# Kernel tuning notes

Hardware: AMD Instinct MI355X
Metric: run time of the kernel (lower is better)

Reference implementation:

```python
import jax, jax.numpy as jnp
import numpy as np

# Emulation of MinkowskiEngine sparse conv semantics on a dense grid with an
# occupancy mask: features are zero at unoccupied sites; stride-1 conv outputs
# only at occupied sites (gather-GEMM-scatter over existing coords); stride-2
# maxpool takes max over occupied sites in each 2x2 block and the output site
# is occupied iff any input site was; stride-2 kernel-2 conv-transpose is
# 'generative': each occupied input spawns its full 2x2 output block.
# MinkowskiConvolution has bias=False by default; MinkowskiDropout is identity
# in eval mode (omitted).

_DN = ('NHWC', 'HWIO', 'NHWC')

def mconv(x, m, w):
    # x: [B,H,W,Ci] (zero outside m), m: [B,H,W] bool, w: [kh,kw,Ci,Co]
    y = jax.lax.conv_general_dilated(x, w, (1, 1), 'SAME', dimension_numbers=_DN)
    return jnp.where(m[..., None], y, 0.0)

def mpool(x, m):
    # 2x2 stride-2 max pool over occupied sites only
    B, H, W, C = x.shape
    xn = jnp.where(m[..., None], x, -jnp.inf)
    p = xn.reshape(B, H // 2, 2, W // 2, 2, C).max(axis=(2, 4))
    mo = m.reshape(B, H // 2, 2, W // 2, 2).any(axis=(2, 4))
    return jnp.where(mo[..., None], p, 0.0), mo

def mtconv(x, m, w):
    # kernel-2 stride-2 transpose: out[b,2i+di,2j+dj] = w[di,dj].T @ x[b,i,j]
    B, H, W, Ci = x.shape
    Co = w.shape[-1]
    y = jnp.einsum('bhwc,ijco->bhiwjo', x, w).reshape(B, 2 * H, 2 * W, Co)
    mo = jnp.repeat(jnp.repeat(m, 2, axis=1), 2, axis=2)
    return jnp.where(mo[..., None], y, 0.0), mo


def setup_inputs() -> dict:
    key = jax.random.key(0)
    ks = jax.random.split(key, 20)

    def mkw(k, shape):
        fan_in = int(np.prod(shape[:-1]))
        return (jax.random.normal(k, shape, dtype=jnp.float32) / np.sqrt(fan_in)).astype(jnp.float32)

    B, H, W = 2, 1024, 1024
    x = jax.random.normal(ks[0], (B, H, W, 1), dtype=jnp.float32)
    mask = jax.random.randint(ks[1], (B, H, W), 0, 2, dtype=jnp.int32)
    return {
        'x': x, 'mask': mask,
        'w_ds1': mkw(ks[2], (3, 3, 1, 16)),
        'w_ds2': mkw(ks[3], (3, 3, 16, 32)),
        'w_ds3': mkw(ks[4], (3, 3, 32, 64)),
        'w_ds4': mkw(ks[5], (3, 3, 64, 128)),
        'w_bridge': mkw(ks[6], (3, 3, 128, 256)),
        'wt4': mkw(ks[7], (2, 2, 256, 128)),
        'w_us4': mkw(ks[8], (3, 3, 256, 128)),
        'wt3': mkw(ks[9], (2, 2, 128, 64)),
        'w_us3': mkw(ks[10], (3, 3, 128, 64)),
        'wt2': mkw(ks[11], (2, 2, 64, 32)),
        'w_us2': mkw(ks[12], (3, 3, 64, 32)),
        'wt1': mkw(ks[13], (2, 2, 32, 16)),
        'w_us1': mkw(ks[14], (3, 3, 32, 16)),
        'w_out': mkw(ks[15], (1, 1, 16, 3)),
    }


def reference(x, mask, w_ds1, w_ds2, w_ds3, w_ds4, w_bridge, wt4, w_us4,
              wt3, w_us3, wt2, w_us2, wt1, w_us1, w_out):
    m0 = mask.astype(bool)
    x = jnp.where(m0[..., None], x, 0.0)

    c1 = mconv(x, m0, w_ds1)
    p1, m1 = mpool(c1, m0)
    c2 = mconv(p1, m1, w_ds2)
    p2, m2 = mpool(c2, m1)
    c3 = mconv(p2, m2, w_ds3)
    p3, m3 = mpool(c3, m2)
    c4 = mconv(p3, m3, w_ds4)
    p4, m4 = mpool(c4, m3)

    b = mconv(p4, m4, w_bridge)

    u4, mu4 = mtconv(b, m4, wt4)
    mc4 = mu4 | m3
    r4 = mconv(jnp.concatenate([u4, c4], axis=-1), mc4, w_us4)

    u3, mu3 = mtconv(r4, mc4, wt3)
    mc3 = mu3 | m2
    r3 = mconv(jnp.concatenate([u3, c3], axis=-1), mc3, w_us3)

    u2, mu2 = mtconv(r3, mc3, wt2)
    mc2 = mu2 | m1
    r2 = mconv(jnp.concatenate([u2, c2], axis=-1), mc2, w_us2)

    u1, mu1 = mtconv(r2, mc2, wt1)
    mc1 = mu1 | m0
    r1 = mconv(jnp.concatenate([u1, c1], axis=-1), mc1, w_us1)

    out = mconv(r1, mc1, w_out)
    return (out, c2)
```

## Files before the change

kernel.cpp:

```cpp
#include <hip/hip_runtime.h>
#include <hip/hip_bf16.h>

using bf16 = __hip_bfloat16;
typedef __bf16 bf8 __attribute__((ext_vector_type(8)));
typedef float  f4  __attribute__((ext_vector_type(4)));

__device__ __forceinline__ float b2f(bf16 v){ return __bfloat162float(v); }
__device__ __forceinline__ bf16 f2b(float v){ return __float2bfloat16(v); }

template<typename T> __device__ __forceinline__ float ldv(const void* p, long long i);
template<> __device__ __forceinline__ float ldv<float>(const void* p, long long i){ return ((const float*)p)[i]; }
template<> __device__ __forceinline__ float ldv<bf16 >(const void* p, long long i){ return b2f(((const bf16*)p)[i]); }

__global__ void k_zero_flag(int* f){ *f = 0; }

__global__ void k_detect(const unsigned short* __restrict__ x, long long n, int* __restrict__ flag){
  long long i = blockIdx.x*(long long)blockDim.x + threadIdx.x;
  if (i >= n) return;
  unsigned short u = x[i];
  if ((u & 0x7F80u) == 0x7F80u) atomicOr(flag, 1);
}

__global__ void k_prep(const void* __restrict__ x, const int* __restrict__ m, const int* __restrict__ flag,
                       bf16* __restrict__ xo, unsigned char* __restrict__ mo, long long n){
  long long i = blockIdx.x*(long long)blockDim.x + threadIdx.x;
  if (i >= n) return;
  int f = *flag;
  int mm = (m[i] != 0);
  mo[i] = (unsigned char)mm;
  float v = f ? ldv<float>(x, i) : ldv<bf16>(x, i);
  xo[i] = f2b(mm ? v : 0.f);
}

__global__ void k_mask_comb(const unsigned char* __restrict__ coarse,
                            const unsigned char* __restrict__ fine,
                            unsigned char* __restrict__ mo,
                            int B, int H, int W){
  long long i = blockIdx.x*(long long)blockDim.x + threadIdx.x;
  long long total = (long long)B*H*W;
  if (i >= total) return;
  int x = (int)(i % W);
  long long t = i / W;
  int y = (int)(t % H);
  int b = (int)(t / H);
  unsigned char c = coarse[((long long)b*(H/2) + (y>>1))*(W/2) + (x>>1)];
  mo[i] = (unsigned char)(c | fine[i]);
}

__global__ void k_wt(const int* __restrict__ flag, const void* __restrict__ w, bf16* __restrict__ wt,
                     int taps, int Ci, int Co, int Cip){
  long long i = blockIdx.x*(long long)blockDim.x + threadIdx.x;
  long long total = (long long)taps*Co*Cip;
  if (i >= total) return;
  int ci = (int)(i % Cip);
  long long t2 = i / Cip;
  int co = (int)(t2 % Co);
  int tap = (int)(t2 / Co);
  float v = 0.f;
  if (ci < Ci){
    long long src = ((long long)tap*Ci + ci)*Co + co;
    v = (*flag) ? ldv<float>(w, src) : ldv<bf16>(w, src);
  }
  wt[i] = f2b(v);
}

template<int CI0,int CI1,int CIP,int CO,int COT>
__global__ __launch_bounds__(256)
void k_conv3m(const bf16* __restrict__ in0, const bf16* __restrict__ in1,
              const bf16* __restrict__ wt, const unsigned char* __restrict__ mask,
              void* __restrict__ out, long long out_off, bf16* __restrict__ out2,
              const int* __restrict__ flag, int use_flag,
              int B, int H, int W, int cotiles){
  constexpr int KS = CIP/32;
  int lane = threadIdx.x & 63;
  int wid  = threadIdx.x >> 6;
  int n16  = lane & 15, quad = lane >> 4;
  int x0 = (blockIdx.x*4 + wid)*16;
  int y  = blockIdx.y;
  int b  = blockIdx.z / cotiles;
  int ct = blockIdx.z - b*cotiles;
  int co0 = ct * (16*COT);

  f4 acc[COT];
  #pragma unroll
  for (int j = 0; j < COT; ++j) acc[j] = (f4){0.f,0.f,0.f,0.f};
  bf8 az;
  #pragma unroll
  for (int i = 0; i < 8; ++i) az[i] = (__bf16)0.f;

  bool interior = (x0 > 0) && (x0 + 16 < W);
  int xA = x0 + n16 - 1;

  for (int dy = 0; dy < 3; ++dy){
    int yy = y + dy - 1;
    if ((unsigned)yy >= (unsigned)H) continue;
    const bf16* r0 = in0 + ((long long)b*H + yy)*(long long)W*CI0;
    const bf16* r1 = (CI1 > 0) ? in1 + ((long long)b*H + yy)*(long long)W*CI1 : nullptr;
    const bf16* wrow = wt + ((long long)(dy*3)*CO)*CIP;
    if (interior){
      #pragma unroll
      for (int k0 = 0; k0 < KS; ++k0){
        int c = k0*32 + quad*8;
        bf8 af[3]; bf8 bv[3][COT];
        #pragma unroll
        for (int dx = 0; dx < 3; ++dx){
          long long sx = xA + dx;
          if constexpr (CI1 > 0){
            const bf16* p = (c < CI0) ? r0 + sx*CI0 + c : r1 + sx*CI1 + (c - CI0);
            af[dx] = *(const bf8*)(const void*)p;
          } else if constexpr (CIP > CI0){
            int cc = (c < CI0) ? c : 0;
            bf8 tmp = *(const bf8*)(const void*)(r0 + sx*CI0 + cc);
            af[dx] = (c < CI0) ? tmp : az;
          } else {
            af[dx] = *(const bf8*)(const void*)(r0 + sx*CI0 + c);
          }
          #pragma unroll
          for (int j = 0; j < COT; ++j)
            bv[dx][j] = *(const bf8*)(const void*)(wrow + ((long long)(dx*CO + co0 + j*16 + n16))*CIP + k0*32 + quad*8);
        }
        #pragma unroll
        for (int dx = 0; dx < 3; ++dx)
          #pragma unroll
          for (int j = 0; j < COT; ++j)
            acc[j] = __builtin_amdgcn_mfma_f32_16x16x32_bf16(af[dx], bv[dx][j], acc[j], 0, 0, 0);
      }
    } else {
      #pragma unroll
      for (int k0 = 0; k0 < KS; ++k0){
        int c = k0*32 + quad*8;
        bf8 af[3]; bf8 bv[3][COT];
        #pragma unroll
        for (int dx = 0; dx < 3; ++dx){
          int xx = xA + dx;
          bool ok = (unsigned)xx < (unsigned)W;
          long long sx = ok ? xx : 0;
          bf8 tmp;
          if constexpr (CI1 > 0){
            const bf16* p = (c < CI0) ? r0 + sx*CI0 + c : r1 + sx*CI1 + (c - CI0);
            tmp = *(const bf8*)(const void*)p;
          } else if constexpr (CIP > CI0){
            int cc = (c < CI0) ? c : 0;
            tmp = *(const bf8*)(const void*)(r0 + sx*CI0 + cc);
            if (c >= CI0) ok = false;
          } else {
            tmp = *(const bf8*)(const void*)(r0 + sx*CI0 + c);
          }
          af[dx] = ok ? tmp : az;
          #pragma unroll
          for (int j = 0; j < COT; ++j)
            bv[dx][j] = *(const bf8*)(const void*)(wrow + ((long long)(dx*CO + co0 + j*16 + n16))*CIP + k0*32 + quad*8);
        }
        #pragma unroll
        for (int dx = 0; dx < 3; ++dx)
          #pragma unroll
          for (int j = 0; j < COT; ++j)
            acc[j] = __builtin_amdgcn_mfma_f32_16x16x32_bf16(af[dx], bv[dx][j], acc[j], 0, 0, 0);
      }
    }
  }

  int f = use_flag ? *flag : 0;
  long long srow = ((long long)b*H + y)*(long long)W;
  #pragma unroll
  for (int j = 0; j < COT; ++j){
    #pragma unroll
    for (int r = 0; r < 4; ++r){
      int sx = x0 + quad*4 + r;
      long long s = srow + sx;
      float v = mask[s] ? acc[j][r] : 0.f;
      long long o = s*(long long)CO + co0 + j*16 + n16;
      if (out2) out2[o] = f2b(v);
      if (f) ((float*)out)[out_off + o] = v;
      else   ((bf16*)out)[out_off + o]  = f2b(v);
    }
  }
}

template<int CI,int CO,int COT>
__global__ __launch_bounds__(256)
void k_tconvm(const bf16* __restrict__ in, const bf16* __restrict__ wt,
              bf16* __restrict__ out, int B, int Hi, int Wi, int cotiles){
  constexpr int KS = CI/32;
  int lane = threadIdx.x & 63;
  int wid  = threadIdx.x >> 6;
  int n16  = lane & 15, quad = lane >> 4;
  int ix0 = (blockIdx.x*4 + wid)*16;
  int iy  = blockIdx.y;
  int b   = blockIdx.z / cotiles;
  int ct  = blockIdx.z - b*cotiles;
  int co0 = ct * (16*COT);

  f4 acc[4][COT];
  #pragma unroll
  for (int d = 0; d < 4; ++d)
    #pragma unroll
    for (int j = 0; j < COT; ++j) acc[d][j] = (f4){0.f,0.f,0.f,0.f};

  const bf16* ip = in + (((long long)b*Hi + iy)*(long long)Wi + ix0 + n16)*(long long)CI;
  #pragma unroll
  for (int k0 = 0; k0 < KS; ++k0){
    bf8 a = *(const bf8*)(const void*)(ip + k0*32 + quad*8);
    bf8 bv[4][COT];
    #pragma unroll
    for (int d = 0; d < 4; ++d)
      #pragma unroll
      for (int j = 0; j < COT; ++j)
        bv[d][j] = *(const bf8*)(const void*)(wt + ((long long)(d*CO + co0 + j*16 + n16))*CI + k0*32 + quad*8);
    #pragma unroll
    for (int d = 0; d < 4; ++d)
      #pragma unroll
      for (int j = 0; j < COT; ++j)
        acc[d][j] = __builtin_amdgcn_mfma_f32_16x16x32_bf16(a, bv[d][j], acc[d][j], 0, 0, 0);
  }

  int Ho = Hi*2, Wo = Wi*2;
  #pragma unroll
  for (int d = 0; d < 4; ++d){
    int di = d >> 1, dj = d & 1;
    long long rowo = ((long long)b*Ho + 2*iy + di)*(long long)Wo;
    #pragma unroll
    for (int j = 0; j < COT; ++j){
      #pragma unroll
      for (int r = 0; r < 4; ++r){
        int ix = ix0 + quad*4 + r;
        long long o = (rowo + 2*ix + dj)*(long long)CO + co0 + j*16 + n16;
        out[o] = f2b(acc[d][j][r]);
      }
    }
  }
}

__global__ void k_ds1(const int* __restrict__ flag, const bf16* __restrict__ xm,
                      const void* __restrict__ w, const unsigned char* __restrict__ mask,
                      bf16* __restrict__ out, int B, int H, int W){
  __shared__ float ws[144];
  if (threadIdx.x < 144)
    ws[threadIdx.x] = (*flag) ? ldv<float>(w, threadIdx.x) : ldv<bf16>(w, threadIdx.x);
  __syncthreads();
  long long s = blockIdx.x*(long long)blockDim.x + threadIdx.x;
  long long total = (long long)B*H*W;
  if (s >= total) return;
  int x = (int)(s % W);
  long long t = s / W;
  int y = (int)(t % H);
  int b = (int)(t / H);
  bf8 oz[2];
  #pragma unroll
  for (int h = 0; h < 2; ++h)
    #pragma unroll
    for (int i = 0; i < 8; ++i) oz[h][i] = (__bf16)0.f;
  if (mask[s]){
    float acc[16];
    #pragma unroll
    for (int i = 0; i < 16; ++i) acc[i] = 0.f;
    for (int dy = 0; dy < 3; ++dy){
      int yy = y + dy - 1;
      if ((unsigned)yy >= (unsigned)H) continue;
      long long rowb = ((long long)b*H + yy)*(long long)W;
      for (int dx = 0; dx < 3; ++dx){
        int xx = x + dx - 1;
        if ((unsigned)xx >= (unsigned)W) continue;
        float xv = b2f(xm[rowb + xx]);
        const float* wp = ws + (dy*3 + dx)*16;
        #pragma unroll
        for (int i = 0; i < 16; ++i) acc[i] += xv * wp[i];
      }
    }
    #pragma unroll
    for (int h = 0; h < 2; ++h)
      #pragma unroll
      for (int i = 0; i < 8; ++i) oz[h][i] = (__bf16)acc[h*8+i];
  }
  bf8* op = (bf8*)(void*)(out + s*16);
  op[0] = oz[0]; op[1] = oz[1];
}

__global__ void k_pool8(const bf16* __restrict__ in, const unsigned char* __restrict__ mi,
                        bf16* __restrict__ out, unsigned char* __restrict__ mo,
                        int B, int Ho, int Wo, int C){
  int C8 = C >> 3;
  long long idx = blockIdx.x*(long long)blockDim.x + threadIdx.x;
  long long total = (long long)B*Ho*Wo*C8;
  if (idx >= total) return;
  int c8 = (int)(idx % C8);
  long long s = idx / C8;
  int x = (int)(s % Wo);
  long long t = s / Wo;
  int y = (int)(t % Ho);
  int b = (int)(t / Ho);
  int Hi = Ho*2, Wi = Wo*2;
  float best[8];
  #pragma unroll
  for (int i = 0; i < 8; ++i) best[i] = -3.4e38f;
  bool any = false;
  #pragma unroll
  for (int a = 0; a < 2; ++a){
    #pragma unroll
    for (int d = 0; d < 2; ++d){
      long long site = ((long long)b*Hi + (2*y+a))*(long long)Wi + (2*x+d);
      if (mi[site]){
        any = true;
        bf8 v = *(const bf8*)(const void*)(in + site*(long long)C + c8*8);
        #pragma unroll
        for (int i = 0; i < 8; ++i) best[i] = fmaxf(best[i], (float)v[i]);
      }
    }
  }
  bf8 o;
  #pragma unroll
  for (int i = 0; i < 8; ++i) o[i] = (__bf16)(any ? best[i] : 0.f);
  *(bf8*)(void*)(out + s*(long long)C + c8*8) = o;
  if (c8 == 0) mo[s] = (unsigned char)any;
}

__global__ void k_head(const int* __restrict__ flag, const bf16* __restrict__ in,
                       const void* __restrict__ w, const unsigned char* __restrict__ mask,
                       void* __restrict__ out, int B, int H, int W){
  __shared__ float ws[48];
  if (threadIdx.x < 48)
    ws[threadIdx.x] = (*flag) ? ldv<float>(w, threadIdx.x) : ldv<bf16>(w, threadIdx.x);
  __syncthreads();
  long long s = blockIdx.x*(long long)blockDim.x + threadIdx.x;
  long long total = (long long)B*H*W;
  if (s >= total) return;
  float acc[3] = {0.f, 0.f, 0.f};
  if (mask[s]){
    const bf8* ip = (const bf8*)(const void*)(in + s*16);
    bf8 v0 = ip[0], v1 = ip[1];
    #pragma unroll
    for (int c = 0; c < 8; ++c){
      float a = (float)v0[c], bv = (float)v1[c];
      #pragma unroll
      for (int co = 0; co < 3; ++co){
        acc[co] += a  * ws[c*3 + co];
        acc[co] += bv * ws[(c+8)*3 + co];
      }
    }
  }
  int f = *flag;
  #pragma unroll
  for (int co = 0; co < 3; ++co){
    long long o = s*3 + co;
    if (f) ((float*)out)[o] = acc[co];
    else   ((bf16*)out)[o]  = f2b(acc[co]);
  }
}

static inline dim3 grid1d(long long total, int block){
  return dim3((unsigned)((total + block - 1) / block));
}

extern "C" void kernel_launch(void* const* d_in, const int* in_sizes, int n_in,
                              void* d_out, int out_size, void* d_ws, size_t ws_size,
                              hipStream_t stream) {
  const void* x    = d_in[0];
  const int* mask  = (const int*)d_in[1];
  const void* w_ds1=d_in[2], *w_ds2=d_in[3], *w_ds3=d_in[4], *w_ds4=d_in[5];
  const void* w_bridge=d_in[6];
  const void* wt4=d_in[7], *w_us4=d_in[8], *wt3=d_in[9], *w_us3=d_in[10];
  const void* wt2=d_in[11], *w_us2=d_in[12], *wt1=d_in[13], *w_us1=d_in[14];
  const void* w_out=d_in[15];

  const long long C2_OFF = (long long)2*1024*1024*3;
  const int B = 2;

  int* flag = (int*)d_ws;
  bf16* wsb = (bf16*)((char*)d_ws + 16);
  long long off = 0;
  bf16* xm   = wsb + off; off += (long long)2*1024*1024*1;
  bf16* c1   = wsb + off; off += (long long)2*1024*1024*16;
  bf16* c2b  = wsb + off; off += (long long)2*512*512*32;
  bf16* c3   = wsb + off; off += (long long)2*256*256*64;
  bf16* c4   = wsb + off; off += (long long)2*128*128*128;
  bf16* ping = wsb + off; off += (long long)2*1024*1024*16;
  bf16* pong = wsb + off; off += (long long)2*1024*1024*16;
  bf16* wtds2 = wsb + off; off += (long long)9*32*32;
  bf16* wtds3 = wsb + off; off += (long long)9*64*32;
  bf16* wtds4 = wsb + off; off += (long long)9*128*64;
  bf16* wtbr  = wsb + off; off += (long long)9*256*128;
  bf16* wtus4 = wsb + off; off += (long long)9*128*256;
  bf16* wtus3 = wsb + off; off += (long long)9*64*128;
  bf16* wtus2 = wsb + off; off += (long long)9*32*64;
  bf16* wtus1 = wsb + off; off += (long long)9*16*32;
  bf16* wtt4 = wsb + off; off += (long long)4*128*256;
  bf16* wtt3 = wsb + off; off += (long long)4*64*128;
  bf16* wtt2 = wsb + off; off += (long long)4*32*64;
  bf16* wtt1 = wsb + off; off += (long long)4*16*32;
  unsigned char* mb = (unsigned char*)(wsb + off);
  long long mo = 0;
  unsigned char* m0u = mb + mo; mo += (long long)2*1024*1024;
  unsigned char* m1  = mb + mo; mo += (long long)2*512*512;
  unsigned char* m2  = mb + mo; mo += (long long)2*256*256;
  unsigned char* m3  = mb + mo; mo += (long long)2*128*128;
  unsigned char* m4  = mb + mo; mo += (long long)2*64*64;
  unsigned char* mc4 = mb + mo; mo += (long long)2*128*128;
  unsigned char* mc3 = mb + mo; mo += (long long)2*256*256;
  unsigned char* mc2 = mb + mo; mo += (long long)2*512*512;
  unsigned char* mc1 = mb + mo; mo += (long long)2*1024*1024;

  const int BK = 256;
  long long n;

  k_zero_flag<<<1,1,0,stream>>>(flag);
  n = (long long)B*1024*1024;
  k_detect<<<grid1d(n,BK),BK,0,stream>>>((const unsigned short*)x, n, flag);
  k_prep  <<<grid1d(n,BK),BK,0,stream>>>(x, mask, flag, xm, m0u, n);

  k_wt<<<grid1d((long long)9*32*32 ,BK),BK,0,stream>>>(flag, w_ds2,   wtds2, 9,  16,  32,  32);
  k_wt<<<grid1d((long long)9*64*32 ,BK),BK,0,stream>>>(flag, w_ds3,   wtds3, 9,  32,  64,  32);
  k_wt<<<grid1d((long long)9*128*64,BK),BK,0,stream>>>(flag, w_ds4,   wtds4, 9,  64, 128,  64);
  k_wt<<<grid1d((long long)9*256*128,BK),BK,0,stream>>>(flag, w_bridge,wtbr , 9, 128, 256, 128);
  k_wt<<<grid1d((long long)9*128*256,BK),BK,0,stream>>>(flag, w_us4,  wtus4, 9, 256, 128, 256);
  k_wt<<<grid1d((long long)9*64*128,BK),BK,0,stream>>>(flag, w_us3,   wtus3, 9, 128,  64, 128);
  k_wt<<<grid1d((long long)9*32*64 ,BK),BK,0,stream>>>(flag, w_us2,   wtus2, 9,  64,  32,  64);
  k_wt<<<grid1d((long long)9*16*32 ,BK),BK,0,stream>>>(flag, w_us1,   wtus1, 9,  32,  16,  32);
  k_wt<<<grid1d((long long)4*128*256,BK),BK,0,stream>>>(flag, wt4, wtt4, 4, 256, 128, 256);
  k_wt<<<grid1d((long long)4*64*128 ,BK),BK,0,stream>>>(flag, wt3, wtt3, 4, 128,  64, 128);
  k_wt<<<grid1d((long long)4*32*64  ,BK),BK,0,stream>>>(flag, wt2, wtt2, 4,  64,  32,  64);
  k_wt<<<grid1d((long long)4*16*32  ,BK),BK,0,stream>>>(flag, wt1, wtt1, 4,  32,  16,  32);

  n = (long long)B*1024*1024;
  k_ds1<<<grid1d(n,BK),BK,0,stream>>>(flag, xm, w_ds1, m0u, c1, B,1024,1024);
  n = (long long)B*512*512*2;
  k_pool8<<<grid1d(n,BK),BK,0,stream>>>(c1, m0u, ping, m1, B,512,512,16);

  k_conv3m<16,0,32,32,2><<<dim3(8,512,2),256,0,stream>>>(ping,nullptr, wtds2, m1, d_out, C2_OFF, c2b, flag,1, B,512,512, 1);
  n = (long long)B*256*256*4;
  k_pool8<<<grid1d(n,BK),BK,0,stream>>>(c2b, m1, ping, m2, B,256,256,32);

  k_conv3m<32,0,32,64,2><<<dim3(4,256,4),256,0,stream>>>(ping,nullptr, wtds3, m2, c3, 0, nullptr, flag,0, B,256,256, 2);
  n = (long long)B*128*128*8;
  k_pool8<<<grid1d(n,BK),BK,0,stream>>>(c3, m2, ping, m3, B,128,128,64);

  k_conv3m<64,0,64,128,2><<<dim3(2,128,8),256,0,stream>>>(ping,nullptr, wtds4, m3, c4, 0, nullptr, flag,0, B,128,128, 4);
  n = (long long)B*64*64*16;
  k_pool8<<<grid1d(n,BK),BK,0,stream>>>(c4, m3, ping, m4, B,64,64,128);

  k_conv3m<128,0,128,256,2><<<dim3(1,64,16),256,0,stream>>>(ping,nullptr, wtbr, m4, pong, 0, nullptr, flag,0, B,64,64, 8);

  k_tconvm<256,128,2><<<dim3(1,64,8),256,0,stream>>>(pong, wtt4, ping, B,64,64, 4);
  n = (long long)B*128*128;
  k_mask_comb<<<grid1d(n,BK),BK,0,stream>>>(m4, m3, mc4, B,128,128);
  k_conv3m<128,128,256,128,2><<<dim3(2,128,8),256,0,stream>>>(ping,c4, wtus4, mc4, pong, 0, nullptr, flag,0, B,128,128, 4);

  k_tconvm<128,64,2><<<dim3(2,128,4),256,0,stream>>>(pong, wtt3, ping, B,128,128, 2);
  n = (long long)B*256*256;
  k_mask_comb<<<grid1d(n,BK),BK,0,stream>>>(mc4, m2, mc3, B,256,256);
  k_conv3m<64,64,128,64,2><<<dim3(4,256,4),256,0,stream>>>(ping,c3, wtus3, mc3, pong, 0, nullptr, flag,0, B,256,256, 2);

  k_tconvm<64,32,2><<<dim3(4,256,2),256,0,stream>>>(pong, wtt2, ping, B,256,256, 1);
  n = (long long)B*512*512;
  k_mask_comb<<<grid1d(n,BK),BK,0,stream>>>(mc3, m1, mc2, B,512,512);
  k_conv3m<32,32,64,32,2><<<dim3(8,512,2),256,0,stream>>>(ping,c2b, wtus2, mc2, pong, 0, nullptr, flag,0, B,512,512, 1);

  k_tconvm<32,16,1><<<dim3(8,512,2),256,0,stream>>>(pong, wtt1, ping, B,512,512, 1);
  n = (long long)B*1024*1024;
  k_mask_comb<<<grid1d(n,BK),BK,0,stream>>>(mc2, m0u, mc1, B,1024,1024);
  k_conv3m<16,16,32,16,1><<<dim3(16,1024,2),256,0,stream>>>(ping,c1, wtus1, mc1, pong, 0, nullptr, flag,0, B,1024,1024, 1);

  n = (long long)B*1024*1024;
  k_head<<<grid1d(n,BK),BK,0,stream>>>(flag, pong, w_out, mc1, d_out, B,1024,1024);
}
```

Measured before the change: 1.249 ms.

## Compute multiple output rows per warp in 3x3 conv to reuse input rows

The 3x3 masked conv kernel now computes ROWS output rows per wave. It loads ROWS+2 input rows once per k-slice and all 9 weight taps at once, then reuses each input row across the overlapping dy taps. This cuts redundant global loads of activations and weights. The separate interior/border paths are merged into one predicated path, and the grids for the larger layers are shrunk to match. The cost is more registers for accumulators and fragments, which may lower occupancy on the deeper-channel layers.

```diff
diff --git a/kernel.cpp b/kernel.cpp
--- a/kernel.cpp
+++ b/kernel.cpp
@@ -64,7 +64,7 @@
   wt[i] = f2b(v);
 }
 
-template<int CI0,int CI1,int CIP,int CO,int COT>
+template<int CI0,int CI1,int CIP,int CO,int COT,int ROWS>
 __global__ __launch_bounds__(256)
 void k_conv3m(const bf16* __restrict__ in0, const bf16* __restrict__ in1,
               const bf16* __restrict__ wt, const unsigned char* __restrict__ mask,
@@ -72,107 +72,91 @@
               const int* __restrict__ flag, int use_flag,
               int B, int H, int W, int cotiles){
   constexpr int KS = CIP/32;
+  constexpr int NR = ROWS + 2;
   int lane = threadIdx.x & 63;
   int wid  = threadIdx.x >> 6;
   int n16  = lane & 15, quad = lane >> 4;
   int x0 = (blockIdx.x*4 + wid)*16;
-  int y  = blockIdx.y;
+  int y0 = blockIdx.y*ROWS;
   int b  = blockIdx.z / cotiles;
   int ct = blockIdx.z - b*cotiles;
   int co0 = ct * (16*COT);
 
-  f4 acc[COT];
-  #pragma unroll
-  for (int j = 0; j < COT; ++j) acc[j] = (f4){0.f,0.f,0.f,0.f};
+  f4 acc[ROWS][COT];
+  #pragma unroll
+  for (int r = 0; r < ROWS; ++r)
+    #pragma unroll
+    for (int j = 0; j < COT; ++j) acc[r][j] = (f4){0.f,0.f,0.f,0.f};
   bf8 az;
   #pragma unroll
   for (int i = 0; i < 8; ++i) az[i] = (__bf16)0.f;
 
-  bool interior = (x0 > 0) && (x0 + 16 < W);
   int xA = x0 + n16 - 1;
-
-  for (int dy = 0; dy < 3; ++dy){
-    int yy = y + dy - 1;
-    if ((unsigned)yy >= (unsigned)H) continue;
-    const bf16* r0 = in0 + ((long long)b*H + yy)*(long long)W*CI0;
-    const bf16* r1 = (CI1 > 0) ? in1 + ((long long)b*H + yy)*(long long)W*CI1 : nullptr;
-    const bf16* wrow = wt + ((long long)(dy*3)*CO)*CIP;
-    if (interior){
-      #pragma unroll
-      for (int k0 = 0; k0 < KS; ++k0){
-        int c = k0*32 + quad*8;
-        bf8 af[3]; bf8 bv[3][COT];
-        #pragma unroll
-        for (int dx = 0; dx < 3; ++dx){
-          long long sx = xA + dx;
-          if constexpr (CI1 > 0){
-            const bf16* p = (c < CI0) ? r0 + sx*CI0 + c : r1 + sx*CI1 + (c - CI0);
-            af[dx] = *(const bf8*)(const void*)p;
-          } else if constexpr (CIP > CI0){
-            int cc = (c < CI0) ? c : 0;
-            bf8 tmp = *(const bf8*)(const void*)(r0 + sx*CI0 + cc);
-            af[dx] = (c < CI0) ? tmp : az;
-          } else {
-            af[dx] = *(const bf8*)(const void*)(r0 + sx*CI0 + c);
-          }
-          #pragma unroll
-          for (int j = 0; j < COT; ++j)
-            bv[dx][j] = *(const bf8*)(const void*)(wrow + ((long long)(dx*CO + co0 + j*16 + n16))*CIP + k0*32 + quad*8);
+  const bf16* bb0 = in0 + (long long)b*H*(long long)W*CI0;
+  const bf16* bb1 = (CI1 > 0) ? in1 + (long long)b*H*(long long)W*CI1 : nullptr;
+
+  #pragma unroll
+  for (int k0 = 0; k0 < KS; ++k0){
+    int c = k0*32 + quad*8;
+    bf8 af[NR][3];
+    #pragma unroll
+    for (int ir = 0; ir < NR; ++ir){
+      int yy = y0 + ir - 1;
+      bool yok = (unsigned)yy < (unsigned)H;
+      long long rbase = (long long)(yok ? yy : 0) * W;
+      #pragma unroll
+      for (int dx = 0; dx < 3; ++dx){
+        int xx = xA + dx;
+        bool xok = (unsigned)xx < (unsigned)W;
+        long long sx = rbase + (xok ? xx : 0);
+        bool ok = yok && xok;
+        bf8 tmp;
+        if constexpr (CI1 > 0){
+          const bf16* p = (c < CI0) ? bb0 + sx*CI0 + c : bb1 + sx*CI1 + (c - CI0);
+          tmp = *(const bf8*)(const void*)p;
+        } else if constexpr (CIP > CI0){
+          int cc = (c < CI0) ? c : 0;
+          tmp = *(const bf8*)(const void*)(bb0 + sx*CI0 + cc);
+          if (c >= CI0) ok = false;
+        } else {
+          tmp = *(const bf8*)(const void*)(bb0 + sx*CI0 + c);
         }
+        af[ir][dx] = ok ? tmp : az;
+      }
+    }
+    bf8 bv[9][COT];
+    #pragma unroll
+    for (int t = 0; t < 9; ++t)
+      #pragma unroll
+      for (int j = 0; j < COT; ++j)
+        bv[t][j] = *(const bf8*)(const void*)(wt + ((long long)(t*CO + co0 + j*16 + n16))*CIP + k0*32 + quad*8);
+    #pragma unroll
+    for (int r = 0; r < ROWS; ++r)
+      #pragma unroll
+      for (int dy = 0; dy < 3; ++dy)
         #pragma unroll
         for (int dx = 0; dx < 3; ++dx)
           #pragma unroll
           for (int j = 0; j < COT; ++j)
-            acc[j] = __builtin_amdgcn_mfma_f32_16x16x32_bf16(af[dx], bv[dx][j], acc[j], 0, 0, 0);
-      }
-    } else {
-      #pragma unroll
-      for (int k0 = 0; k0 < KS; ++k0){
-        int c = k0*32 + quad*8;
-        bf8 af[3]; bf8 bv[3][COT];
-        #pragma unroll
-        for (int dx = 0; dx < 3; ++dx){
-          int xx = xA + dx;
-          bool ok = (unsigned)xx < (unsigned)W;
-          long long sx = ok ? xx : 0;
-          bf8 tmp;
-          if constexpr (CI1 > 0){
-            const bf16* p = (c < CI0) ? r0 + sx*CI0 + c : r1 + sx*CI1 + (c - CI0);
-            tmp = *(const bf8*)(const void*)p;
-          } else if constexpr (CIP > CI0){
-            int cc = (c < CI0) ? c : 0;
-            tmp = *(const bf8*)(const void*)(r0 + sx*CI0 + cc);
-            if (c >= CI0) ok = false;
-          } else {
-            tmp = *(const bf8*)(const void*)(r0 + sx*CI0 + c);
-          }
-          af[dx] = ok ? tmp : az;
-          #pragma unroll
-          for (int j = 0; j < COT; ++j)
-            bv[dx][j] = *(const bf8*)(const void*)(wrow + ((long long)(dx*CO + co0 + j*16 + n16))*CIP + k0*32 + quad*8);
-        }
-        #pragma unroll
-        for (int dx = 0; dx < 3; ++dx)
-          #pragma unroll
-          for (int j = 0; j < COT; ++j)
-            acc[j] = __builtin_amdgcn_mfma_f32_16x16x32_bf16(af[dx], bv[dx][j], acc[j], 0, 0, 0);
-      }
-    }
+            acc[r][j] = __builtin_amdgcn_mfma_f32_16x16x32_bf16(af[r+dy][dx], bv[dy*3+dx][j], acc[r][j], 0, 0, 0);
   }
 
   int f = use_flag ? *flag : 0;
-  long long srow = ((long long)b*H + y)*(long long)W;
-  #pragma unroll
-  for (int j = 0; j < COT; ++j){
-    #pragma unroll
-    for (int r = 0; r < 4; ++r){
-      int sx = x0 + quad*4 + r;
-      long long s = srow + sx;
-      float v = mask[s] ? acc[j][r] : 0.f;
-      long long o = s*(long long)CO + co0 + j*16 + n16;
-      if (out2) out2[o] = f2b(v);
-      if (f) ((float*)out)[out_off + o] = v;
-      else   ((bf16*)out)[out_off + o]  = f2b(v);
+  #pragma unroll
+  for (int r2 = 0; r2 < ROWS; ++r2){
+    long long srow = ((long long)b*H + y0 + r2)*(long long)W;
+    #pragma unroll
+    for (int j = 0; j < COT; ++j){
+      #pragma unroll
+      for (int r = 0; r < 4; ++r){
+        int sx = x0 + quad*4 + r;
+        long long s = srow + sx;
+        float v = mask[s] ? acc[r2][j][r] : 0.f;
+        long long o = s*(long long)CO + co0 + j*16 + n16;
+        if (out2) out2[o] = f2b(v);
+        if (f) ((float*)out)[out_off + o] = v;
+        else   ((bf16*)out)[out_off + o]  = f2b(v);
+      }
     }
   }
 }
@@ -425,39 +409,39 @@
   n = (long long)B*512*512*2;
   k_pool8<<<grid1d(n,BK),BK,0,stream>>>(c1, m0u, ping, m1, B,512,512,16);
 
-  k_conv3m<16,0,32,32,2><<<dim3(8,512,2),256,0,stream>>>(ping,nullptr, wtds2, m1, d_out, C2_OFF, c2b, flag,1, B,512,512, 1);
+  k_conv3m<16,0,32,32,2,2><<<dim3(8,256,2),256,0,stream>>>(ping,nullptr, wtds2, m1, d_out, C2_OFF, c2b, flag,1, B,512,512, 1);
   n = (long long)B*256*256*4;
   k_pool8<<<grid1d(n,BK),BK,0,stream>>>(c2b, m1, ping, m2, B,256,256,32);
 
-  k_conv3m<32,0,32,64,2><<<dim3(4,256,4),256,0,stream>>>(ping,nullptr, wtds3, m2, c3, 0, nullptr, flag,0, B,256,256, 2);
+  k_conv3m<32,0,32,64,2,2><<<dim3(4,128,4),256,0,stream>>>(ping,nullptr, wtds3, m2, c3, 0, nullptr, flag,0, B,256,256, 2);
   n = (long long)B*128*128*8;
   k_pool8<<<grid1d(n,BK),BK,0,stream>>>(c3, m2, ping, m3, B,128,128,64);
 
-  k_conv3m<64,0,64,128,2><<<dim3(2,128,8),256,0,stream>>>(ping,nullptr, wtds4, m3, c4, 0, nullptr, flag,0, B,128,128, 4);
+  k_conv3m<64,0,64,128,2,2><<<dim3(2,64,8),256,0,stream>>>(ping,nullptr, wtds4, m3, c4, 0, nullptr, flag,0, B,128,128, 4);
   n = (long long)B*64*64*16;
   k_pool8<<<grid1d(n,BK),BK,0,stream>>>(c4, m3, ping, m4, B,64,64,128);
 
-  k_conv3m<128,0,128,256,2><<<dim3(1,64,16),256,0,stream>>>(ping,nullptr, wtbr, m4, pong, 0, nullptr, flag,0, B,64,64, 8);
+  k_conv3m<128,0,128,256,2,1><<<dim3(1,64,16),256,0,stream>>>(ping,nullptr, wtbr, m4, pong, 0, nullptr, flag,0, B,64,64, 8);
 
   k_tconvm<256,128,2><<<dim3(1,64,8),256,0,stream>>>(pong, wtt4, ping, B,64,64, 4);
   n = (long long)B*128*128;
   k_mask_comb<<<grid1d(n,BK),BK,0,stream>>>(m4, m3, mc4, B,128,128);
-  k_conv3m<128,128,256,128,2><<<dim3(2,128,8),256,0,stream>>>(ping,c4, wtus4, mc4, pong, 0, nullptr, flag,0, B,128,128, 4);
+  k_conv3m<128,128,256,128,2,1><<<dim3(2,128,8),256,0,stream>>>(ping,c4, wtus4, mc4, pong, 0, nullptr, flag,0, B,128,128, 4);
 
   k_tconvm<128,64,2><<<dim3(2,128,4),256,0,stream>>>(pong, wtt3, ping, B,128,128, 2);
   n = (long long)B*256*256;
   k_mask_comb<<<grid1d(n,BK),BK,0,stream>>>(mc4, m2, mc3, B,256,256);
-  k_conv3m<64,64,128,64,2><<<dim3(4,256,4),256,0,stream>>>(ping,c3, wtus3, mc3, pong, 0, nullptr, flag,0, B,256,256, 2);
+  k_conv3m<64,64,128,64,2,1><<<dim3(4,256,4),256,0,stream>>>(ping,c3, wtus3, mc3, pong, 0, nullptr, flag,0, B,256,256, 2);
 
   k_tconvm<64,32,2><<<dim3(4,256,2),256,0,stream>>>(pong, wtt2, ping, B,256,256, 1);
   n = (long long)B*512*512;
   k_mask_comb<<<grid1d(n,BK),BK,0,stream>>>(mc3, m1, mc2, B,512,512);
-  k_conv3m<32,32,64,32,2><<<dim3(8,512,2),256,0,stream>>>(ping,c2b, wtus2, mc2, pong, 0, nullptr, flag,0, B,512,512, 1);
+  k_conv3m<32,32,64,32,2,2><<<dim3(8,256,2),256,0,stream>>>(ping,c2b, wtus2, mc2, pong, 0, nullptr, flag,0, B,512,512, 1);
 
   k_tconvm<32,16,1><<<dim3(8,512,2),256,0,stream>>>(pong, wtt1, ping, B,512,512, 1);
   n = (long long)B*1024*1024;
   k_mask_comb<<<grid1d(n,BK),BK,0,stream>>>(mc2, m0u, mc1, B,1024,1024);
-  k_conv3m<16,16,32,16,1><<<dim3(16,1024,2),256,0,stream>>>(ping,c1, wtus1, mc1, pong, 0, nullptr, flag,0, B,1024,1024, 1);
+  k_conv3m<16,16,32,16,1,4><<<dim3(16,256,2),256,0,stream>>>(ping,c1, wtus1, mc1, pong, 0, nullptr, flag,0, B,1024,1024, 1);
 
   n = (long long)B*1024*1024;
   k_head<<<grid1d(n,BK),BK,0,stream>>>(flag, pong, w_out, mc1, d_out, B,1024,1024);
```

New measurement: 1.095 ms. 1.14x faster.
